# Kernel tuning notes

Hardware: AMD Instinct MI355X
Metric: run time of the kernel (lower is better)

Reference implementation:

```python
import jax, jax.numpy as jnp
import numpy as np

V, MAXLEN, D, I, C, L, S = 32000, 4096, 1024, 4096, 1024, 4, 4096


def setup_inputs() -> dict:
    key = jax.random.key(0)
    ks = jax.random.split(key, 20)
    sd = 0.02
    inp = {
        "input_indices": jax.random.randint(ks[0], (S,), 0, V),
        "emb": jax.random.normal(ks[1], (V, D), jnp.float32) * sd,
        "pos": jax.random.normal(ks[2], (MAXLEN, D), jnp.float32) * sd,
        "Wq": jax.random.normal(ks[3], (L, D, I), jnp.float32) * sd,
        "bq": jnp.zeros((L, I), jnp.float32),
        "Wk": jax.random.normal(ks[4], (L, D, I), jnp.float32) * sd,
        "bk": jnp.zeros((L, I), jnp.float32),
        "Wv": jax.random.normal(ks[5], (L, D, I), jnp.float32) * sd,
        "bv": jnp.zeros((L, I), jnp.float32),
        "Wo": jax.random.normal(ks[6], (L, I, D), jnp.float32) * sd,
        "bo": jnp.zeros((L, D), jnp.float32),
        "W1": jax.random.normal(ks[7], (L, D, I), jnp.float32) * sd,
        "b1": jnp.zeros((L, I), jnp.float32),
        "W2": jax.random.normal(ks[8], (L, I, D), jnp.float32) * sd,
        "b2": jnp.zeros((L, D), jnp.float32),
        "Wout": jax.random.normal(ks[9], (D, C), jnp.float32) * sd,
        "bout": jnp.zeros((C,), jnp.float32),
    }
    return inp


def reference(input_indices, emb, pos, Wq, bq, Wk, bk, Wv, bv, Wo, bo, W1, b1, W2, b2, Wout, bout):
    s = input_indices.shape[0]
    x = emb[input_indices] + pos[:s]  # [S, D]
    causal_mask = jnp.triu(jnp.ones((s, s), bool), k=1)  # True above diagonal -> masked
    scale = 1.0 / np.sqrt(Wq.shape[-1]).astype(np.float32)

    def layer(x, p):
        wq, bq_, wk, bk_, wv, bv_, wo, bo_, w1, b1_, w2, b2_ = p
        q = x @ wq + bq_  # [S, I]
        k = x @ wk + bk_
        v = x @ wv + bv_
        scores = (q @ k.T) * scale  # [S, S]
        scores = jnp.where(causal_mask, -jnp.inf, scores)
        attn = jax.nn.softmax(scores, axis=-1)
        r = x + (attn @ v) @ wo + bo_  # residual + attention output projection
        f = jnp.maximum(r @ w1 + b1_, 0.0) @ w2 + b2_  # ReLU FFN
        return r + f, attn

    x, attention_maps = jax.lax.scan(
        layer, x, (Wq, bq, Wk, bk, Wv, bv, Wo, bo, W1, b1, W2, b2)
    )
    logits = x @ Wout + bout  # [S, C]
    log_probs = jax.nn.log_softmax(logits, axis=-1)
    return log_probs, attention_maps  # [S, C], [L, S, S]
```

## Files before the change

### kernel.cpp

```cpp
#include <hip/hip_runtime.h>
#include <stdint.h>
#include <math.h>

#define S_ 4096
#define D_ 1024
#define I_ 4096
#define C_ 1024
#define L_ 4

typedef unsigned short u16;
typedef short bf16x8 __attribute__((ext_vector_type(8)));
typedef float f32x4 __attribute__((ext_vector_type(4)));

__device__ __forceinline__ u16 f2bf(float f) {
  union { float f; uint32_t u; } c; c.f = f;
  return (u16)((c.u + 0x7FFFu + ((c.u >> 16) & 1u)) >> 16);
}

__device__ __forceinline__ void gll16(const void* g, void* l) {
  __builtin_amdgcn_global_load_lds(
      (__attribute__((address_space(1))) void*)(g),
      (__attribute__((address_space(3))) void*)(l), 16, 0, 0);
}

#define BAR() asm volatile("s_barrier" ::: "memory")
#define WAITV(n) asm volatile("s_waitcnt vmcnt(" #n ")" ::: "memory")

__global__ __launch_bounds__(512, 2) void gemm256(
    const u16* __restrict__ A, const u16* __restrict__ Bt,
    const float* __restrict__ bias, const float* __restrict__ resid,
    float* __restrict__ outF, u16* __restrict__ outB,
    int M, int N, int K, float scale, int flags)
{
  extern __shared__ char smem[];
  u16* sA = (u16*)smem;
  u16* sB = (u16*)smem + 32768;

  int orig = blockIdx.x, nwg = gridDim.x;
  int q8 = nwg >> 3, r8 = nwg & 7;
  int xcd = orig & 7, rem = orig >> 3;
  int wg = (xcd < r8 ? xcd * (q8 + 1) : r8 * (q8 + 1) + (xcd - r8) * q8) + rem;

  int br, bc;
  if (flags & 2) {
    br = (int)((sqrtf(8.0f * (float)wg + 1.0f) - 1.0f) * 0.5f);
    while ((br + 1) * (br + 2) / 2 <= wg) ++br;
    while (br * (br + 1) / 2 > wg) --br;
    bc = wg - br * (br + 1) / 2;
  } else {
    int nbx = N / 256;
    br = wg / nbx; bc = wg % nbx;
  }
  int row0 = br * 256, col0 = bc * 256;

  int tid = threadIdx.x, l = tid & 63;
  int w = tid >> 6;
  int wr = w >> 2, wc = w & 3;
  int lrow = l & 15, lq = l >> 4;
  int hb = wc >> 1;
  int rx = (lrow & 7);

  const u16* ap[2]; const u16* bp[2]; int dst[2];
#pragma unroll
  for (int u = 0; u < 2; ++u) {
    int c = u * 512 + tid;
    int row = c >> 3;
    int oct = (c & 7) ^ (row & 7);
    ap[u] = A + (size_t)(row0 + row) * K + oct * 8;
    bp[u] = Bt + (size_t)(col0 + row) * K + oct * 8;
    dst[u] = c * 8;
  }

#define STAGE_A(par, hh, t)                                                     \
  { _Pragma("unroll") for (int u = 0; u < 2; ++u)                               \
      gll16(ap[u] + (size_t)(hh) * 128 * K + (t) * 64,                          \
            &sA[((par) * 2 + (hh)) * 8192 + dst[u]]); }
#define STAGE_B(par, hh, t)                                                     \
  { _Pragma("unroll") for (int u = 0; u < 2; ++u)                               \
      gll16(bp[u] + (size_t)(hh) * 128 * K + (t) * 64,                          \
            &sB[((par) * 2 + (hh)) * 8192 + dst[u]]); }

#define LD_A(DST, par, mh)                                                      \
  { _Pragma("unroll") for (int mi = 0; mi < 4; ++mi)                            \
    _Pragma("unroll") for (int kc = 0; kc < 2; ++kc)                            \
      DST[mi][kc] = *(const bf16x8*)&sA[((par) * 2 + wr) * 8192 +               \
          ((mh) * 64 + mi * 16 + lrow) * 64 + (((kc * 4 + lq) ^ rx) * 8)]; }
#define LD_B(DST, par, nh)                                                      \
  { _Pragma("unroll") for (int nj = 0; nj < 2; ++nj)                            \
    _Pragma("unroll") for (int kc = 0; kc < 2; ++kc)                            \
      DST[nj][kc] = *(const bf16x8*)&sB[((par) * 2 + hb) * 8192 +               \
          ((wc & 1) * 64 + (nh) * 32 + nj * 16 + lrow) * 64 +                   \
          (((kc * 4 + lq) ^ rx) * 8)]; }

  f32x4 acc[8][4];
#pragma unroll
  for (int i = 0; i < 8; ++i)
#pragma unroll
    for (int j = 0; j < 4; ++j) {
      acc[i][j][0] = 0.f; acc[i][j][1] = 0.f; acc[i][j][2] = 0.f; acc[i][j][3] = 0.f;
    }

#define MM(AF, MB, NB)                                                          \
  { __builtin_amdgcn_s_setprio(1);                                             \
    _Pragma("unroll") for (int kc = 0; kc < 2; ++kc)                            \
    _Pragma("unroll") for (int mi = 0; mi < 4; ++mi)                            \
    _Pragma("unroll") for (int nj = 0; nj < 2; ++nj)                            \
      acc[(MB) + mi][(NB) + nj] = __builtin_amdgcn_mfma_f32_16x16x32_bf16(      \
          AF[mi][kc], bfv[nj][kc], acc[(MB) + mi][(NB) + nj], 0, 0, 0);         \
    __builtin_amdgcn_s_setprio(0); }

  int ktiles = K / 64;
  if (flags & 4) { int lim = ((br + 1) * 256) / 64; if (lim < ktiles) ktiles = lim; }

  bf16x8 afA[4][2], afB[4][2], bfv[2][2];

  STAGE_A(0, 0, 0); STAGE_A(0, 1, 0); STAGE_B(0, 0, 0); STAGE_B(0, 1, 0);
  STAGE_A(1, 0, 1); STAGE_A(1, 1, 1); STAGE_B(1, 0, 1);
  WAITV(6);
  BAR();

  for (int t = 0; t < ktiles; ++t) {
    int p = t & 1;
    LD_A(afA, p, 0);
    LD_B(bfv, p, 0);
    LD_A(afB, p, 1);
    if (t + 1 < ktiles) STAGE_B(p ^ 1, 1, t + 1);
    BAR();
    MM(afA, 0, 0);
    BAR();
    if (t + 2 < ktiles) STAGE_A(p, 0, t + 2);
    BAR();
    MM(afB, 4, 0);
    BAR();
    LD_B(bfv, p, 1);
    if (t + 2 < ktiles) STAGE_A(p, 1, t + 2);
    BAR();
    MM(afB, 4, 2);
    BAR();
    if (t + 2 < ktiles) STAGE_B(p, 0, t + 2);
    BAR();
    MM(afA, 0, 2);
    if (t + 2 < ktiles) { WAITV(6); } else { WAITV(0); }
    BAR();
  }
#undef STAGE_A
#undef STAGE_B
#undef LD_A
#undef LD_B
#undef MM

  float biasv[4] = {0.f, 0.f, 0.f, 0.f};
  if (bias) {
#pragma unroll
    for (int j = 0; j < 4; ++j) biasv[j] = bias[col0 + wc * 64 + j * 16 + lrow];
  }
  bool do_relu = (flags & 1) != 0;
#pragma unroll
  for (int i = 0; i < 8; ++i) {
#pragma unroll
    for (int r = 0; r < 4; ++r) {
      int row = row0 + wr * 128 + i * 16 + lq * 4 + r;
      size_t ro = (size_t)row * N;
#pragma unroll
      for (int j = 0; j < 4; ++j) {
        int col = col0 + wc * 64 + j * 16 + lrow;
        float v = acc[i][j][r] * scale + biasv[j];
        if (resid) v += resid[ro + col];
        if (do_relu) v = fmaxf(v, 0.f);
        if (outF) outF[ro + col] = v;
        if (outB) outB[ro + col] = f2bf(v);
      }
    }
  }
}

template <int BM_, int BN_>
__global__ __launch_bounds__(256) void gemm_bt(
    const u16* __restrict__ A, const u16* __restrict__ Bt,
    const float* __restrict__ bias, const float* __restrict__ resid,
    float* __restrict__ outF, u16* __restrict__ outB,
    int M, int N, int K, float scale, int flags)
{
  constexpr int FM = BM_ / 32;
  constexpr int FN = BN_ / 32;
  constexpr int ALOADS = BM_ * 8 / 256;
  constexpr int BLOADS = BN_ * 8 / 256;
  constexpr int WROWS = BM_ / 2;
  constexpr int WCOLS = BN_ / 2;

  int orig = blockIdx.x;
  int nwg = gridDim.x;
  int q8 = nwg >> 3, r8 = nwg & 7;
  int xcd = orig & 7, rem = orig >> 3;
  int wg = (xcd < r8 ? xcd * (q8 + 1) : r8 * (q8 + 1) + (xcd - r8) * q8) + rem;

  int nbx = N / BN_;
  int br = wg / nbx, bc = wg % nbx;

  int tid = threadIdx.x;
  int l = tid & 63, w = tid >> 6;
  int wr = w >> 1, wc = w & 1;
  int lrow = l & 15, lq = l >> 4;
  int row0 = br * BM_, col0 = bc * BN_;

  __shared__ u16 lA[2][BM_ * 64];
  __shared__ u16 lB[2][BN_ * 64];

  const u16* aptr[ALOADS];
  const u16* bptr[BLOADS];
#pragma unroll
  for (int t = 0; t < ALOADS; ++t) {
    int c = t * 256 + tid;
    int row = c >> 3;
    int oct = (c & 7) ^ (row & 7);
    aptr[t] = A + (size_t)(row0 + row) * K + oct * 8;
  }
#pragma unroll
  for (int t = 0; t < BLOADS; ++t) {
    int c = t * 256 + tid;
    int row = c >> 3;
    int oct = (c & 7) ^ (row & 7);
    bptr[t] = Bt + (size_t)(col0 + row) * K + oct * 8;
  }

#define STAGE(b, koff)                                                          \
  {                                                                             \
    _Pragma("unroll") for (int t = 0; t < ALOADS; ++t)                          \
        gll16(aptr[t] + (koff), &lA[b][(t * 256 + tid) * 8]);                   \
    _Pragma("unroll") for (int t = 0; t < BLOADS; ++t)                          \
        gll16(bptr[t] + (koff), &lB[b][(t * 256 + tid) * 8]);                   \
  }

  f32x4 acc[FM][FN];
#pragma unroll
  for (int i = 0; i < FM; ++i)
#pragma unroll
    for (int j = 0; j < FN; ++j) {
      acc[i][j][0] = 0.f; acc[i][j][1] = 0.f; acc[i][j][2] = 0.f; acc[i][j][3] = 0.f;
    }

  int ktiles = K / 64;
  int rxA = lrow & 7;

  STAGE(0, 0);
  __syncthreads();
  int cur = 0;
  for (int kt = 0; kt < ktiles; ++kt) {
    if (kt + 1 < ktiles) STAGE(cur ^ 1, (kt + 1) * 64);
#pragma unroll
    for (int kc = 0; kc < 2; ++kc) {
      int kq = kc * 4 + lq;
      int octA = (kq ^ rxA) * 8;
      bf16x8 af[FM], bfv[FN];
#pragma unroll
      for (int i = 0; i < FM; ++i)
        af[i] = *(const bf16x8*)&lA[cur][(wr * WROWS + i * 16 + lrow) * 64 + octA];
#pragma unroll
      for (int j = 0; j < FN; ++j)
        bfv[j] = *(const bf16x8*)&lB[cur][(wc * WCOLS + j * 16 + lrow) * 64 + octA];
#pragma unroll
      for (int i = 0; i < FM; ++i)
#pragma unroll
        for (int j = 0; j < FN; ++j)
          acc[i][j] = __builtin_amdgcn_mfma_f32_16x16x32_bf16(af[i], bfv[j], acc[i][j], 0, 0, 0);
    }
    __syncthreads();
    cur ^= 1;
  }
#undef STAGE

  float biasv[FN];
#pragma unroll
  for (int j = 0; j < FN; ++j) biasv[j] = 0.f;
  if (bias) {
#pragma unroll
    for (int j = 0; j < FN; ++j) biasv[j] = bias[col0 + wc * WCOLS + j * 16 + lrow];
  }
  bool do_relu = (flags & 1) != 0;
#pragma unroll
  for (int i = 0; i < FM; ++i) {
#pragma unroll
    for (int r = 0; r < 4; ++r) {
      int row = row0 + wr * WROWS + i * 16 + lq * 4 + r;
      size_t ro = (size_t)row * N;
#pragma unroll
      for (int j = 0; j < FN; ++j) {
        int col = col0 + wc * WCOLS + j * 16 + lrow;
        float v = acc[i][j][r] * scale + biasv[j];
        if (resid) v += resid[ro + col];
        if (do_relu) v = fmaxf(v, 0.f);
        if (outF) outF[ro + col] = v;
        if (outB) outB[ro + col] = f2bf(v);
      }
    }
  }
}

struct T6 {
  const float* src[6];
  u16* dst[6];
};

__global__ __launch_bounds__(256) void trans6_f2b(T6 a) {
  __shared__ float tile[32][33];
  int z = blockIdx.z;
  bool big = (z == 3 || z == 5);
  int R = big ? I_ : D_;
  int C = big ? D_ : I_;
  int bid = blockIdx.y * gridDim.x + blockIdx.x;
  int nbx = C / 32;
  int bx = bid % nbx, by = bid / nbx;
  const float* src = a.src[z];
  u16* dst = a.dst[z];
  int c0 = bx * 32, r0 = by * 32;
  int tx = threadIdx.x & 31, ty = threadIdx.x >> 5;
#pragma unroll
  for (int i = 0; i < 32; i += 8)
    tile[ty + i][tx] = src[(size_t)(r0 + ty + i) * C + c0 + tx];
  __syncthreads();
#pragma unroll
  for (int i = 0; i < 32; i += 8)
    dst[(size_t)(c0 + ty + i) * R + r0 + tx] = f2bf(tile[tx][ty + i]);
}

__global__ __launch_bounds__(256) void trans_f2b(const float* __restrict__ src,
                                                 u16* __restrict__ dst, int R, int C)
{
  __shared__ float tile[32][33];
  int c0 = blockIdx.x * 32, r0 = blockIdx.y * 32;
  int tx = threadIdx.x & 31, ty = threadIdx.x >> 5;
#pragma unroll
  for (int i = 0; i < 32; i += 8)
    tile[ty + i][tx] = src[(size_t)(r0 + ty + i) * C + c0 + tx];
  __syncthreads();
#pragma unroll
  for (int i = 0; i < 32; i += 8)
    dst[(size_t)(c0 + ty + i) * R + r0 + tx] = f2bf(tile[tx][ty + i]);
}

__global__ __launch_bounds__(256) void trans_b2b(const u16* __restrict__ src,
                                                 u16* __restrict__ dst, int R, int C)
{
  __shared__ u16 tile[64][68];
  int c0 = blockIdx.x * 64, r0 = blockIdx.y * 64;
  int tx = threadIdx.x & 63, ty = threadIdx.x >> 6;
#pragma unroll
  for (int i = 0; i < 64; i += 4)
    tile[ty + i][tx] = src[(size_t)(r0 + ty + i) * C + c0 + tx];
  __syncthreads();
#pragma unroll
  for (int i = 0; i < 64; i += 4)
    dst[(size_t)(c0 + ty + i) * R + r0 + tx] = tile[tx][ty + i];
}

__global__ __launch_bounds__(256) void embed_k(const int* __restrict__ idx,
                                               const float* __restrict__ emb,
                                               const float* __restrict__ pos,
                                               float* __restrict__ xf, u16* __restrict__ xb)
{
  int s = blockIdx.y;
  int d = blockIdx.x * 256 + threadIdx.x;
  float v = emb[(size_t)idx[s] * D_ + d] + pos[(size_t)s * D_ + d];
  size_t o = (size_t)s * D_ + d;
  xf[o] = v;
  xb[o] = f2bf(v);
}

__global__ __launch_bounds__(256) void softmax_causal(float* __restrict__ att, u16* __restrict__ attB)
{
  int s = blockIdx.x;
  __shared__ float row[S_];
  __shared__ float red[8];
  int tid = threadIdx.x, l = tid & 63, w = tid >> 6;
  int nv = s + 1;
  size_t base = (size_t)s * S_;
  float m = -3.0e38f;
  for (int c = tid; c < nv; c += 256) { float v = att[base + c]; row[c] = v; m = fmaxf(m, v); }
#pragma unroll
  for (int off = 32; off; off >>= 1) m = fmaxf(m, __shfl_xor(m, off, 64));
  if (l == 0) red[w] = m;
  __syncthreads();
  m = fmaxf(fmaxf(red[0], red[1]), fmaxf(red[2], red[3]));
  float sum = 0.f;
  for (int c = tid; c < nv; c += 256) { float e = __expf(row[c] - m); row[c] = e; sum += e; }
#pragma unroll
  for (int off = 32; off; off >>= 1) sum += __shfl_xor(sum, off, 64);
  if (l == 0) red[4 + w] = sum;
  __syncthreads();
  sum = red[4] + red[5] + red[6] + red[7];
  float inv = 1.0f / sum;
  int nb = ((s >> 8) + 1) * 256;
  for (int c = tid; c < S_; c += 256) {
    float p = (c < nv) ? row[c] * inv : 0.0f;
    att[base + c] = p;
    if (c < nb) attB[base + c] = f2bf(p);
  }
}

__global__ __launch_bounds__(256) void logsoftmax_k(const float* __restrict__ logits,
                                                    float* __restrict__ out)
{
  int s = blockIdx.x;
  int tid = threadIdx.x, l = tid & 63, w = tid >> 6;
  __shared__ float red[8];
  size_t base = (size_t)s * C_;
  float v[4];
  float m = -3.0e38f;
#pragma unroll
  for (int k = 0; k < 4; ++k) { v[k] = logits[base + tid + k * 256]; m = fmaxf(m, v[k]); }
#pragma unroll
  for (int off = 32; off; off >>= 1) m = fmaxf(m, __shfl_xor(m, off, 64));
  if (l == 0) red[w] = m;
  __syncthreads();
  m = fmaxf(fmaxf(red[0], red[1]), fmaxf(red[2], red[3]));
  float sum = 0.f;
#pragma unroll
  for (int k = 0; k < 4; ++k) sum += __expf(v[k] - m);
#pragma unroll
  for (int off = 32; off; off >>= 1) sum += __shfl_xor(sum, off, 64);
  if (l == 0) red[4 + w] = sum;
  __syncthreads();
  sum = red[4] + red[5] + red[6] + red[7];
  float lz = logf(sum);
#pragma unroll
  for (int k = 0; k < 4; ++k) out[base + tid + k * 256] = v[k] - m - lz;
}

extern "C" void kernel_launch(void* const* d_in, const int* in_sizes, int n_in,
                              void* d_out, int out_size, void* d_ws, size_t ws_size,
                              hipStream_t stream) {
  (void)in_sizes; (void)n_in; (void)out_size; (void)ws_size;
  const int*   idx  = (const int*)d_in[0];
  const float* emb  = (const float*)d_in[1];
  const float* pos  = (const float*)d_in[2];
  const float* Wq   = (const float*)d_in[3];
  const float* bq   = (const float*)d_in[4];
  const float* Wk   = (const float*)d_in[5];
  const float* bk   = (const float*)d_in[6];
  const float* Wv   = (const float*)d_in[7];
  const float* bv   = (const float*)d_in[8];
  const float* Wo   = (const float*)d_in[9];
  const float* bo   = (const float*)d_in[10];
  const float* W1   = (const float*)d_in[11];
  const float* b1   = (const float*)d_in[12];
  const float* W2   = (const float*)d_in[13];
  const float* b2   = (const float*)d_in[14];
  const float* Wout = (const float*)d_in[15];
  const float* bout = (const float*)d_in[16];
  float* out = (float*)d_out;

  char* ws = (char*)d_ws;
  const size_t MB = 1024ull * 1024ull;
  float* xres  = (float*)(ws + 0);
  u16*  xbf    = (u16*)(ws + 16 * MB);
  u16*  bufQ   = (u16*)(ws + 24 * MB);
  u16*  bufK   = (u16*)(ws + 56 * MB);
  u16*  bufV   = (u16*)(ws + 88 * MB);
  u16*  bufVT  = (u16*)(ws + 120 * MB);
  u16*  attnB  = (u16*)(ws + 152 * MB);
  float* logit = (float*)(ws + 184 * MB);
  u16* WqT   = (u16*)(ws + 200 * MB);
  u16* WkT   = (u16*)(ws + 208 * MB);
  u16* WvT   = (u16*)(ws + 216 * MB);
  u16* WoT   = (u16*)(ws + 224 * MB);
  u16* W1T   = (u16*)(ws + 232 * MB);
  u16* W2T   = (u16*)(ws + 240 * MB);
  u16* WoutT = (u16*)(ws + 248 * MB);

  const float iscale = 1.0f / 64.0f;
  const int LDSB = 131072;
  hipFuncSetAttribute((const void*)gemm256,
                      hipFuncAttributeMaxDynamicSharedMemorySize, LDSB);
  const int G_SQ = (S_ / 256) * (I_ / 256);
  const int G_TRI = (S_ / 256) * (S_ / 256 + 1) / 2;

  embed_k<<<dim3(D_ / 256, S_), 256, 0, stream>>>(idx, emb, pos, xres, xbf);

  for (int layer = 0; layer < L_; ++layer) {
    T6 t6;
    t6.src[0] = Wq + (size_t)layer * D_ * I_; t6.dst[0] = WqT;
    t6.src[1] = Wk + (size_t)layer * D_ * I_; t6.dst[1] = WkT;
    t6.src[2] = Wv + (size_t)layer * D_ * I_; t6.dst[2] = WvT;
    t6.src[3] = Wo + (size_t)layer * I_ * D_; t6.dst[3] = WoT;
    t6.src[4] = W1 + (size_t)layer * D_ * I_; t6.dst[4] = W1T;
    t6.src[5] = W2 + (size_t)layer * I_ * D_; t6.dst[5] = W2T;
    trans6_f2b<<<dim3(128, 32, 6), 256, 0, stream>>>(t6);

    gemm256<<<G_SQ, 512, LDSB, stream>>>(
        xbf, WqT, bq + (size_t)layer * I_, nullptr, nullptr, bufQ, S_, I_, D_, 1.0f, 0);
    gemm256<<<G_SQ, 512, LDSB, stream>>>(
        xbf, WkT, bk + (size_t)layer * I_, nullptr, nullptr, bufK, S_, I_, D_, 1.0f, 0);
    gemm256<<<G_SQ, 512, LDSB, stream>>>(
        xbf, WvT, bv + (size_t)layer * I_, nullptr, nullptr, bufV, S_, I_, D_, 1.0f, 0);

    trans_b2b<<<dim3(I_ / 64, S_ / 64), 256, 0, stream>>>(bufV, bufVT, S_, I_);

    float* attL = out + (size_t)S_ * C_ + (size_t)layer * S_ * S_;
    gemm256<<<G_TRI, 512, LDSB, stream>>>(
        bufQ, bufK, nullptr, nullptr, attL, nullptr, S_, S_, I_, iscale, 2);

    softmax_causal<<<S_, 256, 0, stream>>>(attL, attnB);

    gemm256<<<(S_ / 256) * (I_ / 256), 512, LDSB, stream>>>(
        attnB, bufVT, nullptr, nullptr, nullptr, bufQ, S_, I_, S_, 1.0f, 4);

    gemm_bt<64, 128><<<(S_ / 64) * (D_ / 128), 256, 0, stream>>>(
        bufQ, WoT, bo + (size_t)layer * D_, xres, xres, xbf, S_, D_, I_, 1.0f, 0);

    gemm256<<<G_SQ, 512, LDSB, stream>>>(
        xbf, W1T, b1 + (size_t)layer * I_, nullptr, nullptr, bufK, S_, I_, D_, 1.0f, 1);

    gemm_bt<64, 128><<<(S_ / 64) * (D_ / 128), 256, 0, stream>>>(
        bufK, W2T, b2 + (size_t)layer * D_, xres, xres, xbf, S_, D_, I_, 1.0f, 0);
  }

  trans_f2b<<<dim3(C_ / 32, D_ / 32), 256, 0, stream>>>(Wout, WoutT, D_, C_);
  gemm_bt<64, 128><<<(S_ / 64) * (C_ / 128), 256, 0, stream>>>(
      xbf, WoutT, bout, nullptr, logit, nullptr, S_, C_, D_, 1.0f, 0);
  logsoftmax_k<<<S_, 256, 0, stream>>>(logit, out);
}
```

Measured before the change: 2.467 ms.

## Split-K the QK^T and Wo/W2 GEMMs to raise workgroup counts

The QK^T score GEMM is split into two K halves, each written to its own fp32 buffer, and the softmax sums the two partials when it reads them. The Wo and W2 projections, which previously used a small 64x128 tile kernel, now use the 256x256 MFMA kernel with a 4-way K split into a partial buffer. A vectorised combine kernel then adds bias and residual and writes the fp32 and bf16 outputs. The aim is to give the 256-tile kernel enough workgroups on the narrow-N GEMMs, at the cost of extra partial-sum memory traffic, extra launches and a larger workspace.

```diff
diff --git a/kernel.cpp b/kernel.cpp
--- a/kernel.cpp
+++ b/kernel.cpp
@@ -26,39 +26,26 @@
 #define BAR() asm volatile("s_barrier" ::: "memory")
 #define WAITV(n) asm volatile("s_waitcnt vmcnt(" #n ")" ::: "memory")
 
-__global__ __launch_bounds__(512, 2) void gemm256(
+__device__ __forceinline__ int xcd_swz(int orig, int nwg) {
+  int q8 = nwg >> 3, r8 = nwg & 7;
+  int xcd = orig & 7, rem = orig >> 3;
+  return (xcd < r8 ? xcd * (q8 + 1) : r8 * (q8 + 1) + (xcd - r8) * q8) + rem;
+}
+
+__device__ __forceinline__ void gemm256_body(
+    u16* sA, u16* sB,
     const u16* __restrict__ A, const u16* __restrict__ Bt,
     const float* __restrict__ bias, const float* __restrict__ resid,
     float* __restrict__ outF, u16* __restrict__ outB,
-    int M, int N, int K, float scale, int flags)
-{
-  extern __shared__ char smem[];
-  u16* sA = (u16*)smem;
-  u16* sB = (u16*)smem + 32768;
-
-  int orig = blockIdx.x, nwg = gridDim.x;
-  int q8 = nwg >> 3, r8 = nwg & 7;
-  int xcd = orig & 7, rem = orig >> 3;
-  int wg = (xcd < r8 ? xcd * (q8 + 1) : r8 * (q8 + 1) + (xcd - r8) * q8) + rem;
-
-  int br, bc;
-  if (flags & 2) {
-    br = (int)((sqrtf(8.0f * (float)wg + 1.0f) - 1.0f) * 0.5f);
-    while ((br + 1) * (br + 2) / 2 <= wg) ++br;
-    while (br * (br + 1) / 2 > wg) --br;
-    bc = wg - br * (br + 1) / 2;
-  } else {
-    int nbx = N / 256;
-    br = wg / nbx; bc = wg % nbx;
-  }
-  int row0 = br * 256, col0 = bc * 256;
-
+    int N, int K, float scale, int relu,
+    int row0, int col0, int t0, int t1)
+{
   int tid = threadIdx.x, l = tid & 63;
   int w = tid >> 6;
   int wr = w >> 2, wc = w & 3;
   int lrow = l & 15, lq = l >> 4;
   int hb = wc >> 1;
-  int rx = (lrow & 7);
+  int rx = lrow & 7;
 
   const u16* ap[2]; const u16* bp[2]; int dst[2];
 #pragma unroll
@@ -79,7 +66,6 @@
   { _Pragma("unroll") for (int u = 0; u < 2; ++u)                               \
       gll16(bp[u] + (size_t)(hh) * 128 * K + (t) * 64,                          \
             &sB[((par) * 2 + (hh)) * 8192 + dst[u]]); }
-
 #define LD_A(DST, par, mh)                                                      \
   { _Pragma("unroll") for (int mi = 0; mi < 4; ++mi)                            \
     _Pragma("unroll") for (int kc = 0; kc < 2; ++kc)                            \
@@ -109,38 +95,35 @@
           AF[mi][kc], bfv[nj][kc], acc[(MB) + mi][(NB) + nj], 0, 0, 0);         \
     __builtin_amdgcn_s_setprio(0); }
 
-  int ktiles = K / 64;
-  if (flags & 4) { int lim = ((br + 1) * 256) / 64; if (lim < ktiles) ktiles = lim; }
-
   bf16x8 afA[4][2], afB[4][2], bfv[2][2];
 
-  STAGE_A(0, 0, 0); STAGE_A(0, 1, 0); STAGE_B(0, 0, 0); STAGE_B(0, 1, 0);
-  STAGE_A(1, 0, 1); STAGE_A(1, 1, 1); STAGE_B(1, 0, 1);
+  STAGE_A(0, 0, t0); STAGE_A(0, 1, t0); STAGE_B(0, 0, t0); STAGE_B(0, 1, t0);
+  STAGE_A(1, 0, t0 + 1); STAGE_A(1, 1, t0 + 1); STAGE_B(1, 0, t0 + 1);
   WAITV(6);
   BAR();
 
-  for (int t = 0; t < ktiles; ++t) {
-    int p = t & 1;
+  for (int t = t0; t < t1; ++t) {
+    int p = (t - t0) & 1;
     LD_A(afA, p, 0);
     LD_B(bfv, p, 0);
     LD_A(afB, p, 1);
-    if (t + 1 < ktiles) STAGE_B(p ^ 1, 1, t + 1);
+    if (t + 1 < t1) STAGE_B(p ^ 1, 1, t + 1);
     BAR();
     MM(afA, 0, 0);
     BAR();
-    if (t + 2 < ktiles) STAGE_A(p, 0, t + 2);
+    if (t + 2 < t1) STAGE_A(p, 0, t + 2);
     BAR();
     MM(afB, 4, 0);
     BAR();
     LD_B(bfv, p, 1);
-    if (t + 2 < ktiles) STAGE_A(p, 1, t + 2);
+    if (t + 2 < t1) STAGE_A(p, 1, t + 2);
     BAR();
     MM(afB, 4, 2);
     BAR();
-    if (t + 2 < ktiles) STAGE_B(p, 0, t + 2);
+    if (t + 2 < t1) STAGE_B(p, 0, t + 2);
     BAR();
     MM(afA, 0, 2);
-    if (t + 2 < ktiles) { WAITV(6); } else { WAITV(0); }
+    if (t + 2 < t1) { WAITV(6); } else { WAITV(0); }
     BAR();
   }
 #undef STAGE_A
@@ -154,7 +137,6 @@
 #pragma unroll
     for (int j = 0; j < 4; ++j) biasv[j] = bias[col0 + wc * 64 + j * 16 + lrow];
   }
-  bool do_relu = (flags & 1) != 0;
 #pragma unroll
   for (int i = 0; i < 8; ++i) {
 #pragma unroll
@@ -166,12 +148,84 @@
         int col = col0 + wc * 64 + j * 16 + lrow;
         float v = acc[i][j][r] * scale + biasv[j];
         if (resid) v += resid[ro + col];
-        if (do_relu) v = fmaxf(v, 0.f);
+        if (relu) v = fmaxf(v, 0.f);
         if (outF) outF[ro + col] = v;
         if (outB) outB[ro + col] = f2bf(v);
       }
     }
   }
+}
+
+__global__ __launch_bounds__(512, 2) void gemm256k(
+    const u16* __restrict__ A, const u16* __restrict__ Bt,
+    const float* __restrict__ bias, const float* __restrict__ resid,
+    float* __restrict__ outF, u16* __restrict__ outB,
+    int M, int N, int K, float scale, int flags, int k0, int k1)
+{
+  extern __shared__ char smem[];
+  int wg = xcd_swz(blockIdx.x, gridDim.x);
+  int nbx = N / 256;
+  int br = wg / nbx, bc = wg % nbx;
+  if (flags & 4) { int lim = (br + 1) * 256; if (lim < k1) k1 = lim; }
+  gemm256_body((u16*)smem, (u16*)smem + 32768, A, Bt, bias, resid, outF, outB,
+               N, K, scale, flags & 1, br * 256, bc * 256, k0 / 64, k1 / 64);
+}
+
+__global__ __launch_bounds__(512, 2) void gemm256_tri2(
+    const u16* __restrict__ A, const u16* __restrict__ Bt,
+    float* __restrict__ outF0, float* __restrict__ outF1,
+    int K, float scale)
+{
+  extern __shared__ char smem[];
+  int wg = xcd_swz(blockIdx.x, gridDim.x);
+  int half = gridDim.x >> 1;
+  int chunk = (wg >= half) ? 1 : 0;
+  int tile = wg - chunk * half;
+  int br = (int)((sqrtf(8.0f * (float)tile + 1.0f) - 1.0f) * 0.5f);
+  while ((br + 1) * (br + 2) / 2 <= tile) ++br;
+  while (br * (br + 1) / 2 > tile) --br;
+  int bc = tile - br * (br + 1) / 2;
+  int k0 = chunk ? K / 2 : 0;
+  int k1 = chunk ? K : K / 2;
+  gemm256_body((u16*)smem, (u16*)smem + 32768, A, Bt, nullptr, nullptr,
+               chunk ? outF1 : outF0, nullptr,
+               S_, K, scale, 0, br * 256, bc * 256, k0 / 64, k1 / 64);
+}
+
+__global__ __launch_bounds__(512, 2) void gemm256_ks4(
+    const u16* __restrict__ A, const u16* __restrict__ Bt,
+    float* __restrict__ pOut, int M, int N, int K)
+{
+  extern __shared__ char smem[];
+  int wg = xcd_swz(blockIdx.x, gridDim.x);
+  int chunk = wg & 3;
+  int tile = wg >> 2;
+  int nbx = N / 256;
+  int br = tile / nbx, bc = tile % nbx;
+  float* o = pOut + (size_t)chunk * M * N;
+  int kq = K / 4;
+  gemm256_body((u16*)smem, (u16*)smem + 32768, A, Bt, nullptr, nullptr,
+               o, nullptr, N, K, 1.0f, 0,
+               br * 256, bc * 256, (chunk * kq) / 64, ((chunk + 1) * kq) / 64);
+}
+
+__global__ __launch_bounds__(256) void combine4(
+    const float* __restrict__ p, const float* __restrict__ bias,
+    const float* __restrict__ resid, float* __restrict__ outF,
+    u16* __restrict__ outB, int MN, int N)
+{
+  int i = (blockIdx.x * 256 + threadIdx.x) * 4;
+  f32x4 v = *(const f32x4*)&p[i];
+  v += *(const f32x4*)&p[MN + i];
+  v += *(const f32x4*)&p[2 * MN + i];
+  v += *(const f32x4*)&p[3 * MN + i];
+  int col = i & (N - 1);
+  v += *(const f32x4*)&bias[col];
+  v += *(const f32x4*)&resid[i];
+  *(f32x4*)&outF[i] = v;
+  ushort4 b;
+  b.x = f2bf(v[0]); b.y = f2bf(v[1]); b.z = f2bf(v[2]); b.w = f2bf(v[3]);
+  *(ushort4*)&outB[i] = b;
 }
 
 template <int BM_, int BN_>
@@ -188,12 +242,7 @@
   constexpr int WROWS = BM_ / 2;
   constexpr int WCOLS = BN_ / 2;
 
-  int orig = blockIdx.x;
-  int nwg = gridDim.x;
-  int q8 = nwg >> 3, r8 = nwg & 7;
-  int xcd = orig & 7, rem = orig >> 3;
-  int wg = (xcd < r8 ? xcd * (q8 + 1) : r8 * (q8 + 1) + (xcd - r8) * q8) + rem;
-
+  int wg = xcd_swz(blockIdx.x, gridDim.x);
   int nbx = N / BN_;
   int br = wg / nbx, bc = wg % nbx;
 
@@ -366,7 +415,9 @@
   xb[o] = f2bf(v);
 }
 
-__global__ __launch_bounds__(256) void softmax_causal(float* __restrict__ att, u16* __restrict__ attB)
+__global__ __launch_bounds__(256) void softmax_causal(float* __restrict__ att,
+                                                      const float* __restrict__ attP1,
+                                                      u16* __restrict__ attB)
 {
   int s = blockIdx.x;
   __shared__ float row[S_];
@@ -375,7 +426,10 @@
   int nv = s + 1;
   size_t base = (size_t)s * S_;
   float m = -3.0e38f;
-  for (int c = tid; c < nv; c += 256) { float v = att[base + c]; row[c] = v; m = fmaxf(m, v); }
+  for (int c = tid; c < nv; c += 256) {
+    float v = att[base + c] + attP1[base + c];
+    row[c] = v; m = fmaxf(m, v);
+  }
 #pragma unroll
   for (int off = 32; off; off >>= 1) m = fmaxf(m, __shfl_xor(m, off, 64));
   if (l == 0) red[w] = m;
@@ -466,13 +520,19 @@
   u16* W1T   = (u16*)(ws + 232 * MB);
   u16* W2T   = (u16*)(ws + 240 * MB);
   u16* WoutT = (u16*)(ws + 248 * MB);
+  float* attP1 = (float*)(ws + 256 * MB);
+  float* pK    = (float*)(ws + 320 * MB);
 
   const float iscale = 1.0f / 64.0f;
   const int LDSB = 131072;
-  hipFuncSetAttribute((const void*)gemm256,
+  hipFuncSetAttribute((const void*)gemm256k,
+                      hipFuncAttributeMaxDynamicSharedMemorySize, LDSB);
+  hipFuncSetAttribute((const void*)gemm256_tri2,
+                      hipFuncAttributeMaxDynamicSharedMemorySize, LDSB);
+  hipFuncSetAttribute((const void*)gemm256_ks4,
                       hipFuncAttributeMaxDynamicSharedMemorySize, LDSB);
   const int G_SQ = (S_ / 256) * (I_ / 256);
-  const int G_TRI = (S_ / 256) * (S_ / 256 + 1) / 2;
+  const int G_TRI2 = (S_ / 256) * (S_ / 256 + 1);
 
   embed_k<<<dim3(D_ / 256, S_), 256, 0, stream>>>(idx, emb, pos, xres, xbf);
 
@@ -486,32 +546,40 @@
     t6.src[5] = W2 + (size_t)layer * I_ * D_; t6.dst[5] = W2T;
     trans6_f2b<<<dim3(128, 32, 6), 256, 0, stream>>>(t6);
 
-    gemm256<<<G_SQ, 512, LDSB, stream>>>(
-        xbf, WqT, bq + (size_t)layer * I_, nullptr, nullptr, bufQ, S_, I_, D_, 1.0f, 0);
-    gemm256<<<G_SQ, 512, LDSB, stream>>>(
-        xbf, WkT, bk + (size_t)layer * I_, nullptr, nullptr, bufK, S_, I_, D_, 1.0f, 0);
-    gemm256<<<G_SQ, 512, LDSB, stream>>>(
-        xbf, WvT, bv + (size_t)layer * I_, nullptr, nullptr, bufV, S_, I_, D_, 1.0f, 0);
+    gemm256k<<<G_SQ, 512, LDSB, stream>>>(
+        xbf, WqT, bq + (size_t)layer * I_, nullptr, nullptr, bufQ,
+        S_, I_, D_, 1.0f, 0, 0, D_);
+    gemm256k<<<G_SQ, 512, LDSB, stream>>>(
+        xbf, WkT, bk + (size_t)layer * I_, nullptr, nullptr, bufK,
+        S_, I_, D_, 1.0f, 0, 0, D_);
+    gemm256k<<<G_SQ, 512, LDSB, stream>>>(
+        xbf, WvT, bv + (size_t)layer * I_, nullptr, nullptr, bufV,
+        S_, I_, D_, 1.0f, 0, 0, D_);
 
     trans_b2b<<<dim3(I_ / 64, S_ / 64), 256, 0, stream>>>(bufV, bufVT, S_, I_);
 
     float* attL = out + (size_t)S_ * C_ + (size_t)layer * S_ * S_;
-    gemm256<<<G_TRI, 512, LDSB, stream>>>(
-        bufQ, bufK, nullptr, nullptr, attL, nullptr, S_, S_, I_, iscale, 2);
-
-    softmax_causal<<<S_, 256, 0, stream>>>(attL, attnB);
-
-    gemm256<<<(S_ / 256) * (I_ / 256), 512, LDSB, stream>>>(
-        attnB, bufVT, nullptr, nullptr, nullptr, bufQ, S_, I_, S_, 1.0f, 4);
-
-    gemm_bt<64, 128><<<(S_ / 64) * (D_ / 128), 256, 0, stream>>>(
-        bufQ, WoT, bo + (size_t)layer * D_, xres, xres, xbf, S_, D_, I_, 1.0f, 0);
-
-    gemm256<<<G_SQ, 512, LDSB, stream>>>(
-        xbf, W1T, b1 + (size_t)layer * I_, nullptr, nullptr, bufK, S_, I_, D_, 1.0f, 1);
-
-    gemm_bt<64, 128><<<(S_ / 64) * (D_ / 128), 256, 0, stream>>>(
-        bufK, W2T, b2 + (size_t)layer * D_, xres, xres, xbf, S_, D_, I_, 1.0f, 0);
+    gemm256_tri2<<<G_TRI2, 512, LDSB, stream>>>(bufQ, bufK, attL, attP1, I_, iscale);
+
+    softmax_causal<<<S_, 256, 0, stream>>>(attL, attP1, attnB);
+
+    gemm256k<<<G_SQ, 512, LDSB, stream>>>(
+        attnB, bufVT, nullptr, nullptr, nullptr, bufQ,
+        S_, I_, S_, 1.0f, 4, 0, S_);
+
+    gemm256_ks4<<<(S_ / 256) * (D_ / 256) * 4, 512, LDSB, stream>>>(
+        bufQ, WoT, pK, S_, D_, I_);
+    combine4<<<(S_ * D_) / 1024, 256, 0, stream>>>(
+        pK, bo + (size_t)layer * D_, xres, xres, xbf, S_ * D_, D_);
+
+    gemm256k<<<G_SQ, 512, LDSB, stream>>>(
+        xbf, W1T, b1 + (size_t)layer * I_, nullptr, nullptr, bufK,
+        S_, I_, D_, 1.0f, 1, 0, D_);
+
+    gemm256_ks4<<<(S_ / 256) * (D_ / 256) * 4, 512, LDSB, stream>>>(
+        bufK, W2T, pK, S_, D_, I_);
+    combine4<<<(S_ * D_) / 1024, 256, 0, stream>>>(
+        pK, b2 + (size_t)layer * D_, xres, xres, xbf, S_ * D_, D_);
   }
 
   trans_f2b<<<dim3(C_ / 32, D_ / 32), 256, 0, stream>>>(Wout, WoutT, D_, C_);
```

Result: faster. 2.377 ms (-3.6%).
